# Kernel optimization log

Hardware: AMD Instinct MI355X
Metric: run time of the kernel (lower is better)

Reference implementation:

```python
import jax, jax.numpy as jnp
import numpy as np

NUM_CODES = 8192
LATENT_DIM = 256
BETA = 0.25
EPS_NORM = 1e-12  # F.normalize eps


def setup_inputs() -> dict:
    key = jax.random.key(0)
    k1, k2 = jax.random.split(key)
    z = jax.random.normal(k1, (8, LATENT_DIM, 32, 32), dtype=jnp.float32)
    # embedding initialized uniform(-1/K, 1/K); use that scale for realism
    codebook = jax.random.uniform(k2, (NUM_CODES, LATENT_DIM), dtype=jnp.float32,
                                  minval=-1.0 / NUM_CODES, maxval=1.0 / NUM_CODES)
    return {"z": z, "codebook": codebook}


def reference(z, codebook):
    # forward re-normalizes the codebook rows (F.normalize dim=1)
    norm = jnp.sqrt(jnp.sum(codebook * codebook, axis=1, keepdims=True))
    w = codebook / jnp.maximum(norm, EPS_NORM)                      # [K, D]

    z_perm = jnp.transpose(z, (0, 2, 3, 1))                          # [B, H, W, D]
    B, H, W, D = z_perm.shape
    zf = z_perm.reshape(-1, D)                                       # [N, D]

    # squared euclidean distances: ||z||^2 + ||w||^2 - 2 z w^T
    d = (jnp.sum(zf * zf, axis=1, keepdims=True)
         + jnp.sum(w * w, axis=1)
         - 2.0 * jnp.einsum('nd,kd->nk', zf, w))                     # [N, K]
    idx = jnp.argmin(d, axis=1)                                      # [N] int

    z_q = w[idx].reshape(B, H, W, D)                                 # gather

    # commitment + codebook loss
    loss = (jnp.mean((jax.lax.stop_gradient(z_q) - z_perm) ** 2)
            + BETA * jnp.mean((z_q - jax.lax.stop_gradient(z_perm)) ** 2))

    # straight-through estimator
    z_q = z_perm + jax.lax.stop_gradient(z_q - z_perm)

    # perplexity from codeword usage histogram (== mean of one-hots)
    N = idx.shape[0]
    counts = jnp.zeros((NUM_CODES,), dtype=jnp.float32).at[idx].add(1.0)
    avg_probs = counts / N
    perplexity = jnp.exp(-jnp.sum(avg_probs * jnp.log(avg_probs + 1e-10)))

    z_q = jnp.transpose(z_q, (0, 3, 1, 2))                           # back to NCHW
    return (z_q, idx, loss, perplexity)
```

## Files before the change

### kernel.cpp

```cpp
#include <hip/hip_runtime.h>
#include <hip/hip_bf16.h>
#include <math.h>

#define KC 8192
#define DD 256
#define NP 8192
#define ZQ_ELEMS 2097152
#define MARGIN_S 2.5e-4f
#define NPART 32

#define OFF_ABIG 0u
#define OFF_BBIG 8388608u
#define OFF_NRM  16777216u
#define OFF_WSQ  16809984u
#define OFF_PV1  16875520u
#define OFF_PV2  17924096u
#define OFF_PK1  18972672u
#define OFF_LOSSP 20021248u
#define OFF_HIST 20090880u
#define OFF_PACK 20123648u
#define OFF_LIST 20189184u
#define OFF_NFLG 20221952u

typedef __attribute__((ext_vector_type(8))) short bf16x8;
typedef __attribute__((ext_vector_type(4))) float f32x4;
typedef __attribute__((address_space(3))) void as3_void;
typedef const __attribute__((address_space(1))) void as1_cvoid;

#define GLOAD16(g, l) __builtin_amdgcn_global_load_lds((as1_cvoid*)(g), (as3_void*)(l), 16, 0, 0)

__device__ inline double waveReduceD(double v) {
#pragma unroll
    for (int off = 32; off; off >>= 1) v += __shfl_down(v, off, 64);
    return v;
}

static __device__ inline unsigned short f2bf(float f) {
    __hip_bfloat16 h = __float2bfloat16(f);
    return *(unsigned short*)&h;
}
static __device__ inline float bf2f(unsigned short u) {
    unsigned v = ((unsigned)u) << 16;
    float f;
    __builtin_memcpy(&f, &v, 4);
    return f;
}

__global__ __launch_bounds__(256) void prep(
    const float* __restrict__ cb, const float* __restrict__ z,
    unsigned short* __restrict__ Bbig, unsigned short* __restrict__ Abig,
    float* __restrict__ nrm, float* __restrict__ wsq,
    int* __restrict__ hist, int* __restrict__ nflag) {
    __shared__ float tile[64][65];
    int bid = blockIdx.x, t = threadIdx.x;
    int lane = t & 63, wid = t >> 6;
    if (bid < KC) {
        __shared__ double lred[4];
        __shared__ float mh;
        int k = bid;
        if (k < 32) hist[k * 256 + t] = 0;
        if (k == 32 && t == 0) *nflag = 0;
        float c = cb[k * DD + t];
        double s = waveReduceD((double)c * (double)c);
        if (lane == 0) lred[wid] = s;
        __syncthreads();
        if (t == 0) {
            double tot = lred[0] + lred[1] + lred[2] + lred[3];
            float nf = sqrtf((float)tot);
            mh = fmaxf(nf, 1e-12f);
            nrm[k] = mh;
            wsq[k] = (float)(tot / ((double)mh * (double)mh));
        }
        __syncthreads();
        float wv = c / mh;
        unsigned short hi = f2bf(wv);
        unsigned short lo = f2bf(wv - bf2f(hi));
        Bbig[k * 512 + t] = hi;
        Bbig[k * 512 + 256 + t] = lo;
    } else {
        int zb = bid - KC;
        int b = zb >> 6, ht = (zb >> 2) & 15, dt = zb & 3;
        int hw0 = ht * 64, d0 = dt * 64;
#pragma unroll
        for (int i = 0; i < 16; ++i) {
            int dl = wid * 16 + i;
            tile[dl][lane] = z[(size_t)(b * DD + d0 + dl) * 1024 + hw0 + lane];
        }
        __syncthreads();
#pragma unroll
        for (int i = 0; i < 16; ++i) {
            int nl = wid * 16 + i;
            float v = tile[lane][nl];
            unsigned short hi = f2bf(v);
            unsigned short lo = f2bf(v - bf2f(hi));
            size_t base = (size_t)(b * 1024 + hw0 + nl) * 512 + d0 + lane;
            Abig[base] = hi;
            Abig[base + 256] = lo;
        }
    }
}

__global__ __launch_bounds__(512, 2) void gemm_top2(
    const unsigned short* __restrict__ Abig, const unsigned short* __restrict__ Bbig,
    const float* __restrict__ wsq,
    float* __restrict__ pv1, float* __restrict__ pv2, int* __restrict__ pk1) {
    __shared__ unsigned short sAB[65536];

    int t = threadIdx.x;
    int l = t & 63, w = t >> 6;
    int wm = w >> 2, wn = w & 3;
    int kc0 = blockIdx.y * 256;
    int n0 = blockIdx.x * 256;

    int row0 = t >> 2;
    int lsw = (((t & 3) ^ ((row0 >> 1) & 3)) << 3);
    int subsw = (((l >> 4) ^ ((l >> 1) & 3)) << 3);

#define STAGE(kt_) do {                                                        \
    int p_ = (kt_) >> 3;                                                       \
    int zo_ = (p_ == 2 ? 256 : 0) + ((kt_) & 7) * 32;                          \
    int wo_ = (p_ == 1 ? 256 : 0) + ((kt_) & 7) * 32;                          \
    int b_ = ((kt_) & 3) * 16384;                                              \
    GLOAD16(Bbig + (size_t)(kc0 + row0) * 512 + wo_ + lsw, &sAB[b_ + t * 8]);  \
    GLOAD16(Bbig + (size_t)(kc0 + row0 + 128) * 512 + wo_ + lsw, &sAB[b_ + 4096 + t * 8]); \
    GLOAD16(Abig + (size_t)(n0 + row0) * 512 + zo_ + lsw, &sAB[b_ + 8192 + t * 8]); \
    GLOAD16(Abig + (size_t)(n0 + row0 + 128) * 512 + zo_ + lsw, &sAB[b_ + 12288 + t * 8]); \
} while (0)

#define LDFRAG(bufbase, fa, fb) do {                                           \
    _Pragma("unroll")                                                          \
    for (int mf = 0; mf < 8; ++mf)                                             \
        fa[mf] = *(const bf16x8*)&sAB[(bufbase) + (wm * 128 + mf * 16 + (l & 15)) * 32 + subsw]; \
    _Pragma("unroll")                                                          \
    for (int nf = 0; nf < 4; ++nf)                                             \
        fb[nf] = *(const bf16x8*)&sAB[(bufbase) + 8192 + (wn * 64 + nf * 16 + (l & 15)) * 32 + subsw]; \
} while (0)

#define MFMACL(fa, fb) do {                                                    \
    __builtin_amdgcn_s_setprio(1);                                             \
    _Pragma("unroll")                                                          \
    for (int mf = 0; mf < 8; ++mf)                                             \
        _Pragma("unroll")                                                      \
        for (int nf = 0; nf < 4; ++nf)                                         \
            acc[mf][nf] = __builtin_amdgcn_mfma_f32_16x16x32_bf16(fa[mf], fb[nf], acc[mf][nf], 0, 0, 0); \
    __builtin_amdgcn_s_setprio(0);                                             \
} while (0)

#define WAITBAR(n_) do {                                                       \
    asm volatile("s_waitcnt vmcnt(" #n_ ")" ::: "memory");                     \
    __builtin_amdgcn_s_barrier();                                              \
    asm volatile("" ::: "memory");                                             \
} while (0)

    f32x4 acc[8][4];
#pragma unroll
    for (int mf = 0; mf < 8; ++mf) {
#pragma unroll
        for (int r = 0; r < 4; ++r) {
            float hv = -0.5f * wsq[kc0 + wm * 128 + mf * 16 + ((l >> 4) << 2) + r];
#pragma unroll
            for (int nf = 0; nf < 4; ++nf) acc[mf][nf][r] = hv;
        }
    }

    bf16x8 fa0[8], fb0[4], fa1[8], fb1[4];

    STAGE(0);
    STAGE(1);
    STAGE(2);
    WAITBAR(8);
    LDFRAG(0, fa0, fb0);

    for (int kt = 0; kt < 20; kt += 2) {
        WAITBAR(4);
        LDFRAG(((kt + 1) & 3) * 16384, fa1, fb1);
        STAGE(kt + 3);
        MFMACL(fa0, fb0);
        WAITBAR(4);
        LDFRAG(((kt + 2) & 3) * 16384, fa0, fb0);
        STAGE(kt + 4);
        MFMACL(fa1, fb1);
    }
    WAITBAR(4);
    LDFRAG(1 * 16384, fa1, fb1);
    STAGE(23);
    MFMACL(fa0, fb0);
    WAITBAR(4);
    LDFRAG(2 * 16384, fa0, fb0);
    MFMACL(fa1, fb1);
    WAITBAR(0);
    LDFRAG(3 * 16384, fa1, fb1);
    MFMACL(fa0, fb0);
    MFMACL(fa1, fb1);

    float v1[4], v2[4];
    int k1[4];
#pragma unroll
    for (int nf = 0; nf < 4; ++nf) { v1[nf] = 3.4e38f; v2[nf] = 3.4e38f; k1[nf] = 0; }
#pragma unroll
    for (int mf = 0; mf < 8; ++mf) {
#pragma unroll
        for (int r = 0; r < 4; ++r) {
            int code = kc0 + wm * 128 + mf * 16 + ((l >> 4) << 2) + r;
#pragma unroll
            for (int nf = 0; nf < 4; ++nf) {
                float dv = -acc[mf][nf][r];
                bool lt = dv < v1[nf];
                v2[nf] = fminf(v2[nf], fmaxf(v1[nf], dv));
                v1[nf] = fminf(v1[nf], dv);
                k1[nf] = lt ? code : k1[nf];
            }
        }
    }
#pragma unroll
    for (int nf = 0; nf < 4; ++nf) {
#pragma unroll
        for (int mask = 16; mask <= 32; mask <<= 1) {
            float ov1 = __shfl_xor(v1[nf], mask, 64);
            float ov2 = __shfl_xor(v2[nf], mask, 64);
            int ok1 = __shfl_xor(k1[nf], mask, 64);
            bool take = (ov1 < v1[nf]) || (ov1 == v1[nf] && ok1 < k1[nf]);
            if (take) { v2[nf] = fminf(v1[nf], ov2); v1[nf] = ov1; k1[nf] = ok1; }
            else v2[nf] = fminf(v2[nf], ov1);
        }
    }
    __syncthreads();
    float* sv1 = (float*)sAB;
    float* sv2 = sv1 + 512;
    int* sk1 = (int*)(sv2 + 512);
    if ((l >> 4) == 0) {
#pragma unroll
        for (int nf = 0; nf < 4; ++nf) {
            int col = wn * 64 + nf * 16 + l;
            sv1[col * 2 + wm] = v1[nf];
            sv2[col * 2 + wm] = v2[nf];
            sk1[col * 2 + wm] = k1[nf];
        }
    }
    __syncthreads();
    if (t < 256) {
        float a1 = sv1[t * 2], b1 = sv1[t * 2 + 1];
        float a2 = sv2[t * 2], b2 = sv2[t * 2 + 1];
        int ak = sk1[t * 2], bk = sk1[t * 2 + 1];
        bool tb = (b1 < a1) || (b1 == a1 && bk < ak);
        float w1 = tb ? b1 : a1;
        int wk = tb ? bk : ak;
        float w2 = tb ? fminf(b2, a1) : fminf(a2, b1);
        pv1[blockIdx.y * NP + n0 + t] = w1;
        pv2[blockIdx.y * NP + n0 + t] = w2;
        pk1[blockIdx.y * NP + n0 + t] = wk;
    }
#undef STAGE
#undef LDFRAG
#undef MFMACL
#undef WAITBAR
}

__global__ __launch_bounds__(256) void merge_top2(
    const float* __restrict__ pv1, const float* __restrict__ pv2,
    const int* __restrict__ pk1, int* __restrict__ list, int* __restrict__ nflag,
    unsigned long long* __restrict__ packed) {
    int n = blockIdx.x * 256 + threadIdx.x;
    float gv1 = 3.4e38f, gv2 = 3.4e38f;
    int gk1 = 0;
#pragma unroll
    for (int ct = 0; ct < NPART; ++ct) {
        float v1 = pv1[ct * NP + n];
        if (v1 < gv1) {
            gv2 = fminf(gv1, pv2[ct * NP + n]);
            gv1 = v1;
            gk1 = pk1[ct * NP + n];
        } else {
            gv2 = fminf(gv2, v1);
        }
    }
    int f = (gv2 - gv1 < MARGIN_S) ? 1 : 0;
    packed[n] = f ? 0xFFFFFFFFFFFFFFFFull : (unsigned long long)(unsigned)gk1;
    if (f) {
        int pos = atomicAdd(nflag, 1);
        list[pos] = n;
    }
}

__global__ __launch_bounds__(256) void rescore_par(
    const float* __restrict__ z, const float* __restrict__ cb,
    const float* __restrict__ nrm, const float* __restrict__ wsq,
    const int* __restrict__ list, const int* __restrict__ nflag,
    unsigned long long* __restrict__ packed) {
    __shared__ float sz[256];
    int nf = *nflag;
    int t = threadIdx.x;
    int lane = t & 63, wv = t >> 6;
    for (int ii = blockIdx.x; ii < nf; ii += 64) {
        int n = list[ii];
        int b = n >> 10, hw = n & 1023;
        __syncthreads();
        sz[t] = z[(b * DD + t) * 1024 + hw];
        __syncthreads();
        float4 zr = ((const float4*)sz)[lane];
        double zqd = (double)zr.x * zr.x + (double)zr.y * zr.y
                   + (double)zr.z * zr.z + (double)zr.w * zr.w;
#pragma unroll
        for (int off = 32; off; off >>= 1) zqd += __shfl_xor(zqd, off, 64);
        float zq = (float)zqd;
        unsigned long long best = 0xFFFFFFFFFFFFFFFFull;
        int kbase = blockIdx.y * 256 + wv * 64;
        for (int j = 0; j < 64; ++j) {
            int k = kbase + j;
            float4 cc = *(const float4*)&cb[(size_t)k * DD + lane * 4];
            float p = (zr.x * cc.x + zr.y * cc.y) + (zr.z * cc.z + zr.w * cc.w);
#pragma unroll
            for (int off = 32; off; off >>= 1) p += __shfl_xor(p, off, 64);
            float dot = p / nrm[k];
            float dv = (zq + wsq[k]) - 2.0f * dot;
            unsigned bits = __float_as_uint(dv);
            bits = (bits & 0x80000000u) ? ~bits : (bits | 0x80000000u);
            unsigned long long pk = ((unsigned long long)bits << 32) | (unsigned)k;
            best = best < pk ? best : pk;
        }
        if (lane == 0) atomicMin(packed + n, best);
    }
}

__global__ __launch_bounds__(256) void gather_loss(
    const float* __restrict__ z, const float* __restrict__ cb,
    const float* __restrict__ nrm, const unsigned long long* __restrict__ packed,
    float* __restrict__ out, double* __restrict__ lossp, int* __restrict__ hist) {
    __shared__ double lred[4];
    int t = threadIdx.x;
    int base = (blockIdx.x * 256 + t) * 16;
    double s = 0.0;
#pragma unroll
    for (int q = 0; q < 4; ++q) {
        int e = base + q * 4;
        int b = e >> 18, d = (e >> 10) & 255, hw = e & 1023;
        int n = (b << 10) + hw;
        float4 zv = *(const float4*)&z[e];
        float o[4];
        int ks[4];
#pragma unroll
        for (int j = 0; j < 4; ++j) {
            ks[j] = (int)(packed[n + j] & 0xFFFFFFFFull);
            o[j] = cb[ks[j] * DD + d] / nrm[ks[j]];
        }
        *(float4*)&out[e] = make_float4(o[0], o[1], o[2], o[3]);
        if (d == 0) {
#pragma unroll
            for (int j = 0; j < 4; ++j) {
                out[ZQ_ELEMS + n + j] = (float)ks[j];
                atomicAdd(&hist[ks[j]], 1);
            }
        }
        float d0 = o[0] - zv.x, d1 = o[1] - zv.y, d2 = o[2] - zv.z, d3 = o[3] - zv.w;
        s += (double)(d0 * d0) + (double)(d1 * d1) + (double)(d2 * d2) + (double)(d3 * d3);
    }
    s = waveReduceD(s);
    int lane = t & 63, wid = t >> 6;
    if (lane == 0) lred[wid] = s;
    __syncthreads();
    if (t == 0) lossp[blockIdx.x] = lred[0] + lred[1] + lred[2] + lred[3];
}

__global__ __launch_bounds__(256) void finalize_kernel(
    const int* __restrict__ hist, const double* __restrict__ lossp,
    float* __restrict__ out) {
    __shared__ double lred[4];
    __shared__ double lsum;
    int t = threadIdx.x;
    int lane = t & 63, wid = t >> 6;
    double ls = lossp[t] + lossp[t + 256];
    ls = waveReduceD(ls);
    if (lane == 0) lred[wid] = ls;
    __syncthreads();
    if (t == 0) lsum = lred[0] + lred[1] + lred[2] + lred[3];
    __syncthreads();
    double s = 0.0;
    for (int i = t; i < KC; i += 256) {
        float p = (float)hist[i] * (1.0f / 8192.0f);
        float lg = logf(p + 1e-10f);
        s += (double)(p * lg);
    }
    s = waveReduceD(s);
    if (lane == 0) lred[wid] = s;
    __syncthreads();
    if (t == 0) {
        double tot = lred[0] + lred[1] + lred[2] + lred[3];
        float m = (float)(lsum / (double)ZQ_ELEMS);
        out[ZQ_ELEMS + NP] = m + 0.25f * m;
        out[ZQ_ELEMS + NP + 1] = expf(-(float)tot);
    }
}

extern "C" void kernel_launch(void* const* d_in, const int* in_sizes, int n_in,
                              void* d_out, int out_size, void* d_ws, size_t ws_size,
                              hipStream_t stream) {
    const float* z = (const float*)d_in[0];
    const float* cb = (const float*)d_in[1];
    float* out = (float*)d_out;
    char* ws = (char*)d_ws;

    unsigned short* Abig = (unsigned short*)(ws + OFF_ABIG);
    unsigned short* Bbig = (unsigned short*)(ws + OFF_BBIG);
    float* nrm = (float*)(ws + OFF_NRM);
    float* wsq = (float*)(ws + OFF_WSQ);
    float* pv1 = (float*)(ws + OFF_PV1);
    float* pv2 = (float*)(ws + OFF_PV2);
    int* pk1 = (int*)(ws + OFF_PK1);
    int* hist = (int*)(ws + OFF_HIST);
    double* lossp = (double*)(ws + OFF_LOSSP);
    unsigned long long* packed = (unsigned long long*)(ws + OFF_PACK);
    int* list = (int*)(ws + OFF_LIST);
    int* nflag = (int*)(ws + OFF_NFLG);

    prep<<<KC + 512, 256, 0, stream>>>(cb, z, Bbig, Abig, nrm, wsq, hist, nflag);
    gemm_top2<<<dim3(32, NPART), 512, 0, stream>>>(Abig, Bbig, wsq, pv1, pv2, pk1);
    merge_top2<<<NP / 256, 256, 0, stream>>>(pv1, pv2, pk1, list, nflag, packed);
    rescore_par<<<dim3(64, 32), 256, 0, stream>>>(z, cb, nrm, wsq, list, nflag, packed);
    gather_loss<<<ZQ_ELEMS / (256 * 16), 256, 0, stream>>>(z, cb, nrm, packed, out, lossp, hist);
    finalize_kernel<<<1, 256, 0, stream>>>(hist, lossp, out);
}
```

Measured before the change: 207.5 us.

## Merge top-2 partials with 64-bit atomics and fuse finalize into gather

The GEMM epilogue now folds each block's top-1/top-2 candidates straight into per-row 64-bit atomicMin slots, using a monotone float-to-uint key. This removes the separate merge kernel and the partial-result buffers. Rescore now reads the ambiguity flag itself instead of using a compacted list. The finalize kernel is folded into the gather kernel with a last-block-done counter. Prep also handles four codebook rows per block, one wave each, with vectorized loads and stores. Together these cut two kernel launches and some global traffic, at the cost of atomic contention in the GEMM epilogue and a per-block scan over all rows in rescore.

```diff
diff --git a/kernel.cpp b/kernel.cpp
--- a/kernel.cpp
+++ b/kernel.cpp
@@ -7,20 +7,17 @@
 #define NP 8192
 #define ZQ_ELEMS 2097152
 #define MARGIN_S 2.5e-4f
-#define NPART 32
 
 #define OFF_ABIG 0u
 #define OFF_BBIG 8388608u
 #define OFF_NRM  16777216u
 #define OFF_WSQ  16809984u
-#define OFF_PV1  16875520u
-#define OFF_PV2  17924096u
-#define OFF_PK1  18972672u
-#define OFF_LOSSP 20021248u
-#define OFF_HIST 20090880u
-#define OFF_PACK 20123648u
-#define OFF_LIST 20189184u
-#define OFF_NFLG 20221952u
+#define OFF_P    16842752u
+#define OFF_P2   16908288u
+#define OFF_R    16973824u
+#define OFF_LOSSP 17039360u
+#define OFF_HIST 17043456u
+#define OFF_DONE 17076224u
 
 typedef __attribute__((ext_vector_type(8))) short bf16x8;
 typedef __attribute__((ext_vector_type(4))) float f32x4;
@@ -45,40 +42,52 @@
     __builtin_memcpy(&f, &v, 4);
     return f;
 }
+static __device__ inline unsigned mono(float f) {
+    unsigned b = __float_as_uint(f);
+    return (b & 0x80000000u) ? ~b : (b | 0x80000000u);
+}
+static __device__ inline float invmono(unsigned u) {
+    unsigned b = (u & 0x80000000u) ? (u & 0x7FFFFFFFu) : ~u;
+    return __uint_as_float(b);
+}
 
 __global__ __launch_bounds__(256) void prep(
     const float* __restrict__ cb, const float* __restrict__ z,
     unsigned short* __restrict__ Bbig, unsigned short* __restrict__ Abig,
-    float* __restrict__ nrm, float* __restrict__ wsq,
-    int* __restrict__ hist, int* __restrict__ nflag) {
-    __shared__ float tile[64][65];
+    float* __restrict__ nrm, float* __restrict__ wsq, int* __restrict__ hist,
+    unsigned long long* __restrict__ P, unsigned long long* __restrict__ P2,
+    unsigned long long* __restrict__ R, unsigned int* __restrict__ done) {
     int bid = blockIdx.x, t = threadIdx.x;
     int lane = t & 63, wid = t >> 6;
-    if (bid < KC) {
-        __shared__ double lred[4];
-        __shared__ float mh;
-        int k = bid;
-        if (k < 32) hist[k * 256 + t] = 0;
-        if (k == 32 && t == 0) *nflag = 0;
-        float c = cb[k * DD + t];
-        double s = waveReduceD((double)c * (double)c);
-        if (lane == 0) lred[wid] = s;
-        __syncthreads();
-        if (t == 0) {
-            double tot = lred[0] + lred[1] + lred[2] + lred[3];
-            float nf = sqrtf((float)tot);
-            mh = fmaxf(nf, 1e-12f);
+    if (bid < 2048) {
+        if (bid < 32) hist[bid * 256 + t] = 0;
+        if (bid == 32 && t == 0) *done = 0u;
+        int k = bid * 4 + wid;
+        float4 c4 = *(const float4*)&cb[(size_t)k * DD + lane * 4];
+        double s = (double)c4.x * c4.x + (double)c4.y * c4.y
+                 + (double)c4.z * c4.z + (double)c4.w * c4.w;
+#pragma unroll
+        for (int off = 32; off; off >>= 1) s += __shfl_xor(s, off, 64);
+        float mh = fmaxf(sqrtf((float)s), 1e-12f);
+        if (lane == 0) {
             nrm[k] = mh;
-            wsq[k] = (float)(tot / ((double)mh * (double)mh));
-        }
-        __syncthreads();
-        float wv = c / mh;
-        unsigned short hi = f2bf(wv);
-        unsigned short lo = f2bf(wv - bf2f(hi));
-        Bbig[k * 512 + t] = hi;
-        Bbig[k * 512 + 256 + t] = lo;
+            wsq[k] = (float)(s / ((double)mh * (double)mh));
+            P[k] = 0xFFFFFFFFFFFFFFFFull;
+            P2[k] = 0xFFFFFFFFFFFFFFFFull;
+            R[k] = 0xFFFFFFFFFFFFFFFFull;
+        }
+        float wv[4] = {c4.x / mh, c4.y / mh, c4.z / mh, c4.w / mh};
+        unsigned short hi[4], lo[4];
+#pragma unroll
+        for (int j = 0; j < 4; ++j) {
+            hi[j] = f2bf(wv[j]);
+            lo[j] = f2bf(wv[j] - bf2f(hi[j]));
+        }
+        *(ushort4*)&Bbig[(size_t)k * 512 + lane * 4] = make_ushort4(hi[0], hi[1], hi[2], hi[3]);
+        *(ushort4*)&Bbig[(size_t)k * 512 + 256 + lane * 4] = make_ushort4(lo[0], lo[1], lo[2], lo[3]);
     } else {
-        int zb = bid - KC;
+        __shared__ float tile[64][65];
+        int zb = bid - 2048;
         int b = zb >> 6, ht = (zb >> 2) & 15, dt = zb & 3;
         int hw0 = ht * 64, d0 = dt * 64;
 #pragma unroll
@@ -103,7 +112,7 @@
 __global__ __launch_bounds__(512, 2) void gemm_top2(
     const unsigned short* __restrict__ Abig, const unsigned short* __restrict__ Bbig,
     const float* __restrict__ wsq,
-    float* __restrict__ pv1, float* __restrict__ pv2, int* __restrict__ pk1) {
+    unsigned long long* __restrict__ P, unsigned long long* __restrict__ P2) {
     __shared__ unsigned short sAB[65536];
 
     int t = threadIdx.x;
@@ -246,9 +255,11 @@
         float w1 = tb ? b1 : a1;
         int wk = tb ? bk : ak;
         float w2 = tb ? fminf(b2, a1) : fminf(a2, b1);
-        pv1[blockIdx.y * NP + n0 + t] = w1;
-        pv2[blockIdx.y * NP + n0 + t] = w2;
-        pk1[blockIdx.y * NP + n0 + t] = wk;
+        int n = n0 + t;
+        unsigned long long x = ((unsigned long long)mono(w1) << 32) | (unsigned)wk;
+        unsigned long long old = atomicMin(&P[n], x);
+        atomicMin(&P2[n], old > x ? old : x);
+        atomicMin(&P2[n], ((unsigned long long)mono(w2) << 32) | 0xFFFFFFFFull);
     }
 #undef STAGE
 #undef LDFRAG
@@ -256,43 +267,25 @@
 #undef WAITBAR
 }
 
-__global__ __launch_bounds__(256) void merge_top2(
-    const float* __restrict__ pv1, const float* __restrict__ pv2,
-    const int* __restrict__ pk1, int* __restrict__ list, int* __restrict__ nflag,
-    unsigned long long* __restrict__ packed) {
-    int n = blockIdx.x * 256 + threadIdx.x;
-    float gv1 = 3.4e38f, gv2 = 3.4e38f;
-    int gk1 = 0;
-#pragma unroll
-    for (int ct = 0; ct < NPART; ++ct) {
-        float v1 = pv1[ct * NP + n];
-        if (v1 < gv1) {
-            gv2 = fminf(gv1, pv2[ct * NP + n]);
-            gv1 = v1;
-            gk1 = pk1[ct * NP + n];
-        } else {
-            gv2 = fminf(gv2, v1);
-        }
-    }
-    int f = (gv2 - gv1 < MARGIN_S) ? 1 : 0;
-    packed[n] = f ? 0xFFFFFFFFFFFFFFFFull : (unsigned long long)(unsigned)gk1;
-    if (f) {
-        int pos = atomicAdd(nflag, 1);
-        list[pos] = n;
-    }
-}
-
 __global__ __launch_bounds__(256) void rescore_par(
     const float* __restrict__ z, const float* __restrict__ cb,
     const float* __restrict__ nrm, const float* __restrict__ wsq,
-    const int* __restrict__ list, const int* __restrict__ nflag,
-    unsigned long long* __restrict__ packed) {
+    const unsigned long long* __restrict__ P, const unsigned long long* __restrict__ P2,
+    unsigned long long* __restrict__ R) {
     __shared__ float sz[256];
-    int nf = *nflag;
+    __shared__ unsigned char fl[128];
     int t = threadIdx.x;
     int lane = t & 63, wv = t >> 6;
-    for (int ii = blockIdx.x; ii < nf; ii += 64) {
-        int n = list[ii];
+    if (t < 128) {
+        int n = blockIdx.x + t * 64;
+        float s1 = invmono((unsigned)(P[n] >> 32));
+        float s2 = invmono((unsigned)(P2[n] >> 32));
+        fl[t] = (s2 - s1 < MARGIN_S) ? 1 : 0;
+    }
+    __syncthreads();
+    for (int ii = 0; ii < 128; ++ii) {
+        if (!fl[ii]) continue;
+        int n = blockIdx.x + ii * 64;
         int b = n >> 10, hw = n & 1023;
         __syncthreads();
         sz[t] = z[(b * DD + t) * 1024 + hw];
@@ -313,21 +306,25 @@
             for (int off = 32; off; off >>= 1) p += __shfl_xor(p, off, 64);
             float dot = p / nrm[k];
             float dv = (zq + wsq[k]) - 2.0f * dot;
-            unsigned bits = __float_as_uint(dv);
-            bits = (bits & 0x80000000u) ? ~bits : (bits | 0x80000000u);
-            unsigned long long pk = ((unsigned long long)bits << 32) | (unsigned)k;
+            unsigned long long pk = ((unsigned long long)mono(dv) << 32) | (unsigned)k;
             best = best < pk ? best : pk;
         }
-        if (lane == 0) atomicMin(packed + n, best);
-    }
-}
-
-__global__ __launch_bounds__(256) void gather_loss(
+        if (lane == 0) atomicMin(&R[n], best);
+    }
+}
+
+__global__ __launch_bounds__(256) void gather_fin(
     const float* __restrict__ z, const float* __restrict__ cb,
-    const float* __restrict__ nrm, const unsigned long long* __restrict__ packed,
-    float* __restrict__ out, double* __restrict__ lossp, int* __restrict__ hist) {
+    const float* __restrict__ nrm,
+    const unsigned long long* __restrict__ P, const unsigned long long* __restrict__ P2,
+    const unsigned long long* __restrict__ R,
+    float* __restrict__ out, double* __restrict__ lossp, int* __restrict__ hist,
+    unsigned int* __restrict__ done) {
     __shared__ double lred[4];
+    __shared__ int amLast;
+    __shared__ double lsum;
     int t = threadIdx.x;
+    int lane = t & 63, wid = t >> 6;
     int base = (blockIdx.x * 256 + t) * 16;
     double s = 0.0;
 #pragma unroll
@@ -340,7 +337,11 @@
         int ks[4];
 #pragma unroll
         for (int j = 0; j < 4; ++j) {
-            ks[j] = (int)(packed[n + j] & 0xFFFFFFFFull);
+            unsigned long long p = P[n + j];
+            float s1 = invmono((unsigned)(p >> 32));
+            float s2 = invmono((unsigned)(P2[n + j] >> 32));
+            unsigned long long wnr = (s2 - s1 < MARGIN_S) ? R[n + j] : p;
+            ks[j] = (int)(wnr & 0xFFFFFFFFull);
             o[j] = cb[ks[j] * DD + d] / nrm[ks[j]];
         }
         *(float4*)&out[e] = make_float4(o[0], o[1], o[2], o[3]);
@@ -355,39 +356,36 @@
         s += (double)(d0 * d0) + (double)(d1 * d1) + (double)(d2 * d2) + (double)(d3 * d3);
     }
     s = waveReduceD(s);
-    int lane = t & 63, wid = t >> 6;
     if (lane == 0) lred[wid] = s;
     __syncthreads();
     if (t == 0) lossp[blockIdx.x] = lred[0] + lred[1] + lred[2] + lred[3];
-}
-
-__global__ __launch_bounds__(256) void finalize_kernel(
-    const int* __restrict__ hist, const double* __restrict__ lossp,
-    float* __restrict__ out) {
-    __shared__ double lred[4];
-    __shared__ double lsum;
-    int t = threadIdx.x;
-    int lane = t & 63, wid = t >> 6;
-    double ls = lossp[t] + lossp[t + 256];
-    ls = waveReduceD(ls);
-    if (lane == 0) lred[wid] = ls;
-    __syncthreads();
-    if (t == 0) lsum = lred[0] + lred[1] + lred[2] + lred[3];
-    __syncthreads();
-    double s = 0.0;
-    for (int i = t; i < KC; i += 256) {
-        float p = (float)hist[i] * (1.0f / 8192.0f);
-        float lg = logf(p + 1e-10f);
-        s += (double)(p * lg);
-    }
-    s = waveReduceD(s);
-    if (lane == 0) lred[wid] = s;
-    __syncthreads();
-    if (t == 0) {
-        double tot = lred[0] + lred[1] + lred[2] + lred[3];
-        float m = (float)(lsum / (double)ZQ_ELEMS);
-        out[ZQ_ELEMS + NP] = m + 0.25f * m;
-        out[ZQ_ELEMS + NP + 1] = expf(-(float)tot);
+    __threadfence();
+    __syncthreads();
+    if (t == 0) amLast = (atomicAdd(done, 1u) == (unsigned)(gridDim.x - 1)) ? 1 : 0;
+    __syncthreads();
+    if (amLast) {
+        __threadfence();
+        double ls = lossp[t] + lossp[t + 256];
+        ls = waveReduceD(ls);
+        if (lane == 0) lred[wid] = ls;
+        __syncthreads();
+        if (t == 0) lsum = lred[0] + lred[1] + lred[2] + lred[3];
+        __syncthreads();
+        double ps = 0.0;
+        for (int i = t; i < KC; i += 256) {
+            float p = (float)hist[i] * (1.0f / 8192.0f);
+            float lg = logf(p + 1e-10f);
+            ps += (double)(p * lg);
+        }
+        ps = waveReduceD(ps);
+        if (lane == 0) lred[wid] = ps;
+        __syncthreads();
+        if (t == 0) {
+            double tot = lred[0] + lred[1] + lred[2] + lred[3];
+            float m = (float)(lsum / (double)ZQ_ELEMS);
+            out[ZQ_ELEMS + NP] = m + 0.25f * m;
+            out[ZQ_ELEMS + NP + 1] = expf(-(float)tot);
+        }
     }
 }
 
@@ -403,19 +401,15 @@
     unsigned short* Bbig = (unsigned short*)(ws + OFF_BBIG);
     float* nrm = (float*)(ws + OFF_NRM);
     float* wsq = (float*)(ws + OFF_WSQ);
-    float* pv1 = (float*)(ws + OFF_PV1);
-    float* pv2 = (float*)(ws + OFF_PV2);
-    int* pk1 = (int*)(ws + OFF_PK1);
+    unsigned long long* P = (unsigned long long*)(ws + OFF_P);
+    unsigned long long* P2 = (unsigned long long*)(ws + OFF_P2);
+    unsigned long long* R = (unsigned long long*)(ws + OFF_R);
+    double* lossp = (double*)(ws + OFF_LOSSP);
     int* hist = (int*)(ws + OFF_HIST);
-    double* lossp = (double*)(ws + OFF_LOSSP);
-    unsigned long long* packed = (unsigned long long*)(ws + OFF_PACK);
-    int* list = (int*)(ws + OFF_LIST);
-    int* nflag = (int*)(ws + OFF_NFLG);
-
-    prep<<<KC + 512, 256, 0, stream>>>(cb, z, Bbig, Abig, nrm, wsq, hist, nflag);
-    gemm_top2<<<dim3(32, NPART), 512, 0, stream>>>(Abig, Bbig, wsq, pv1, pv2, pk1);
-    merge_top2<<<NP / 256, 256, 0, stream>>>(pv1, pv2, pk1, list, nflag, packed);
-    rescore_par<<<dim3(64, 32), 256, 0, stream>>>(z, cb, nrm, wsq, list, nflag, packed);
-    gather_loss<<<ZQ_ELEMS / (256 * 16), 256, 0, stream>>>(z, cb, nrm, packed, out, lossp, hist);
-    finalize_kernel<<<1, 256, 0, stream>>>(hist, lossp, out);
-}
+    unsigned int* done = (unsigned int*)(ws + OFF_DONE);
+
+    prep<<<2560, 256, 0, stream>>>(cb, z, Bbig, Abig, nrm, wsq, hist, P, P2, R, done);
+    gemm_top2<<<dim3(32, 32), 512, 0, stream>>>(Abig, Bbig, wsq, P, P2);
+    rescore_par<<<dim3(64, 32), 256, 0, stream>>>(z, cb, nrm, wsq, P, P2, R);
+    gather_fin<<<512, 256, 0, stream>>>(z, cb, nrm, P, P2, R, out, lossp, hist, done);
+}
```

Result: slower. 293.7 us (+41.6%).

## Loop each GEMM block over four code tiles and vectorize codebook prep

Applied to the files above, without the earlier changes.

The gemm_top2 grid shrinks from 32 to 8 code partitions. Each block now sweeps 1024 codes in one continuous pipelined loop, taking a running top-2 between code tiles, and the partial results are stored row-major per point for the merge. The prep kernel handles four codebook rows per block, one per wave, using float4 loads and shuffle reductions instead of one row per 256-thread block. This cuts block count, per-block pipeline prologue and epilogue overhead, and merge traffic, but leaves fewer blocks (256) to fill the GPU, which may hurt occupancy and load balance.

```diff
diff --git a/kernel.cpp b/kernel.cpp
--- a/kernel.cpp
+++ b/kernel.cpp
@@ -7,7 +7,7 @@
 #define NP 8192
 #define ZQ_ELEMS 2097152
 #define MARGIN_S 2.5e-4f
-#define NPART 32
+#define NPART 8
 
 #define OFF_ABIG 0u
 #define OFF_BBIG 8388608u
@@ -51,34 +51,34 @@
     unsigned short* __restrict__ Bbig, unsigned short* __restrict__ Abig,
     float* __restrict__ nrm, float* __restrict__ wsq,
     int* __restrict__ hist, int* __restrict__ nflag) {
-    __shared__ float tile[64][65];
     int bid = blockIdx.x, t = threadIdx.x;
     int lane = t & 63, wid = t >> 6;
-    if (bid < KC) {
-        __shared__ double lred[4];
-        __shared__ float mh;
-        int k = bid;
-        if (k < 32) hist[k * 256 + t] = 0;
-        if (k == 32 && t == 0) *nflag = 0;
-        float c = cb[k * DD + t];
-        double s = waveReduceD((double)c * (double)c);
-        if (lane == 0) lred[wid] = s;
-        __syncthreads();
-        if (t == 0) {
-            double tot = lred[0] + lred[1] + lred[2] + lred[3];
-            float nf = sqrtf((float)tot);
-            mh = fmaxf(nf, 1e-12f);
+    if (bid < 2048) {
+        if (bid < 32) hist[bid * 256 + t] = 0;
+        if (bid == 32 && t == 0) *nflag = 0;
+        int k = bid * 4 + wid;
+        float4 c4 = *(const float4*)&cb[(size_t)k * DD + lane * 4];
+        double s = (double)c4.x * c4.x + (double)c4.y * c4.y
+                 + (double)c4.z * c4.z + (double)c4.w * c4.w;
+#pragma unroll
+        for (int off = 32; off; off >>= 1) s += __shfl_xor(s, off, 64);
+        float mh = fmaxf(sqrtf((float)s), 1e-12f);
+        if (lane == 0) {
             nrm[k] = mh;
-            wsq[k] = (float)(tot / ((double)mh * (double)mh));
-        }
-        __syncthreads();
-        float wv = c / mh;
-        unsigned short hi = f2bf(wv);
-        unsigned short lo = f2bf(wv - bf2f(hi));
-        Bbig[k * 512 + t] = hi;
-        Bbig[k * 512 + 256 + t] = lo;
+            wsq[k] = (float)(s / ((double)mh * (double)mh));
+        }
+        float wv[4] = {c4.x / mh, c4.y / mh, c4.z / mh, c4.w / mh};
+        unsigned short hi[4], lo[4];
+#pragma unroll
+        for (int j = 0; j < 4; ++j) {
+            hi[j] = f2bf(wv[j]);
+            lo[j] = f2bf(wv[j] - bf2f(hi[j]));
+        }
+        *(ushort4*)&Bbig[(size_t)k * 512 + lane * 4] = make_ushort4(hi[0], hi[1], hi[2], hi[3]);
+        *(ushort4*)&Bbig[(size_t)k * 512 + 256 + lane * 4] = make_ushort4(lo[0], lo[1], lo[2], lo[3]);
     } else {
-        int zb = bid - KC;
+        __shared__ float tile[64][65];
+        int zb = bid - 2048;
         int b = zb >> 6, ht = (zb >> 2) & 15, dt = zb & 3;
         int hw0 = ht * 64, d0 = dt * 64;
 #pragma unroll
@@ -109,20 +109,23 @@
     int t = threadIdx.x;
     int l = t & 63, w = t >> 6;
     int wm = w >> 2, wn = w & 3;
-    int kc0 = blockIdx.y * 256;
+    int kc0 = blockIdx.y * 1024;
     int n0 = blockIdx.x * 256;
 
     int row0 = t >> 2;
     int lsw = (((t & 3) ^ ((row0 >> 1) & 3)) << 3);
     int subsw = (((l >> 4) ^ ((l >> 1) & 3)) << 3);
 
-#define STAGE(kt_) do {                                                        \
-    int p_ = (kt_) >> 3;                                                       \
-    int zo_ = (p_ == 2 ? 256 : 0) + ((kt_) & 7) * 32;                          \
-    int wo_ = (p_ == 1 ? 256 : 0) + ((kt_) & 7) * 32;                          \
-    int b_ = ((kt_) & 3) * 16384;                                              \
-    GLOAD16(Bbig + (size_t)(kc0 + row0) * 512 + wo_ + lsw, &sAB[b_ + t * 8]);  \
-    GLOAD16(Bbig + (size_t)(kc0 + row0 + 128) * 512 + wo_ + lsw, &sAB[b_ + 4096 + t * 8]); \
+#define STAGE(g_) do {                                                         \
+    int ct_ = (g_) / 24;                                                       \
+    int kt_ = (g_) % 24;                                                       \
+    int p_ = kt_ >> 3;                                                         \
+    int zo_ = (p_ == 2 ? 256 : 0) + (kt_ & 7) * 32;                            \
+    int wo_ = (p_ == 1 ? 256 : 0) + (kt_ & 7) * 32;                            \
+    int b_ = ((g_) & 3) * 16384;                                               \
+    int kc_ = kc0 + ct_ * 256;                                                 \
+    GLOAD16(Bbig + (size_t)(kc_ + row0) * 512 + wo_ + lsw, &sAB[b_ + t * 8]);  \
+    GLOAD16(Bbig + (size_t)(kc_ + row0 + 128) * 512 + wo_ + lsw, &sAB[b_ + 4096 + t * 8]); \
     GLOAD16(Abig + (size_t)(n0 + row0) * 512 + zo_ + lsw, &sAB[b_ + 8192 + t * 8]); \
     GLOAD16(Abig + (size_t)(n0 + row0 + 128) * 512 + zo_ + lsw, &sAB[b_ + 12288 + t * 8]); \
 } while (0)
@@ -152,16 +155,43 @@
     asm volatile("" ::: "memory");                                             \
 } while (0)
 
+#define RESETACC(ct_) do {                                                     \
+    _Pragma("unroll")                                                          \
+    for (int mf = 0; mf < 8; ++mf) {                                           \
+        _Pragma("unroll")                                                      \
+        for (int r = 0; r < 4; ++r) {                                          \
+            float hv = -0.5f * wsq[kc0 + (ct_) * 256 + wm * 128 + mf * 16 + ((l >> 4) << 2) + r]; \
+            _Pragma("unroll")                                                  \
+            for (int nf = 0; nf < 4; ++nf) acc[mf][nf][r] = hv;                \
+        }                                                                      \
+    }                                                                          \
+} while (0)
+
+#define EXTRACT(ct_) do {                                                      \
+    _Pragma("unroll")                                                          \
+    for (int mf = 0; mf < 8; ++mf) {                                           \
+        _Pragma("unroll")                                                      \
+        for (int r = 0; r < 4; ++r) {                                          \
+            int code = kc0 + (ct_) * 256 + wm * 128 + mf * 16 + ((l >> 4) << 2) + r; \
+            _Pragma("unroll")                                                  \
+            for (int nf = 0; nf < 4; ++nf) {                                   \
+                float dv = -acc[mf][nf][r];                                    \
+                bool lt = dv < v1[nf];                                         \
+                v2[nf] = fminf(v2[nf], fmaxf(v1[nf], dv));                     \
+                v1[nf] = fminf(v1[nf], dv);                                    \
+                k1[nf] = lt ? code : k1[nf];                                   \
+            }                                                                  \
+        }                                                                      \
+    }                                                                          \
+} while (0)
+
+    float v1[4], v2[4];
+    int k1[4];
+#pragma unroll
+    for (int nf = 0; nf < 4; ++nf) { v1[nf] = 3.4e38f; v2[nf] = 3.4e38f; k1[nf] = 0; }
+
     f32x4 acc[8][4];
-#pragma unroll
-    for (int mf = 0; mf < 8; ++mf) {
-#pragma unroll
-        for (int r = 0; r < 4; ++r) {
-            float hv = -0.5f * wsq[kc0 + wm * 128 + mf * 16 + ((l >> 4) << 2) + r];
-#pragma unroll
-            for (int nf = 0; nf < 4; ++nf) acc[mf][nf][r] = hv;
-        }
-    }
+    RESETACC(0);
 
     bf16x8 fa0[8], fb0[4], fa1[8], fb1[4];
 
@@ -171,47 +201,27 @@
     WAITBAR(8);
     LDFRAG(0, fa0, fb0);
 
-    for (int kt = 0; kt < 20; kt += 2) {
+    for (int g = 0; g < 94; g += 2) {
         WAITBAR(4);
-        LDFRAG(((kt + 1) & 3) * 16384, fa1, fb1);
-        STAGE(kt + 3);
+        LDFRAG(((g + 1) & 3) * 16384, fa1, fb1);
+        STAGE(g + 3);
         MFMACL(fa0, fb0);
         WAITBAR(4);
-        LDFRAG(((kt + 2) & 3) * 16384, fa0, fb0);
-        STAGE(kt + 4);
+        LDFRAG(((g + 2) & 3) * 16384, fa0, fb0);
+        if (g < 92) STAGE(g + 4);
         MFMACL(fa1, fb1);
-    }
-    WAITBAR(4);
-    LDFRAG(1 * 16384, fa1, fb1);
-    STAGE(23);
-    MFMACL(fa0, fb0);
-    WAITBAR(4);
-    LDFRAG(2 * 16384, fa0, fb0);
-    MFMACL(fa1, fb1);
+        if (((g + 1) % 24) == 23) {
+            int ct = (g + 1) / 24;
+            EXTRACT(ct);
+            RESETACC(ct + 1);
+        }
+    }
     WAITBAR(0);
     LDFRAG(3 * 16384, fa1, fb1);
     MFMACL(fa0, fb0);
     MFMACL(fa1, fb1);
-
-    float v1[4], v2[4];
-    int k1[4];
-#pragma unroll
-    for (int nf = 0; nf < 4; ++nf) { v1[nf] = 3.4e38f; v2[nf] = 3.4e38f; k1[nf] = 0; }
-#pragma unroll
-    for (int mf = 0; mf < 8; ++mf) {
-#pragma unroll
-        for (int r = 0; r < 4; ++r) {
-            int code = kc0 + wm * 128 + mf * 16 + ((l >> 4) << 2) + r;
-#pragma unroll
-            for (int nf = 0; nf < 4; ++nf) {
-                float dv = -acc[mf][nf][r];
-                bool lt = dv < v1[nf];
-                v2[nf] = fminf(v2[nf], fmaxf(v1[nf], dv));
-                v1[nf] = fminf(v1[nf], dv);
-                k1[nf] = lt ? code : k1[nf];
-            }
-        }
-    }
+    EXTRACT(3);
+
 #pragma unroll
     for (int nf = 0; nf < 4; ++nf) {
 #pragma unroll
@@ -246,14 +256,16 @@
         float w1 = tb ? b1 : a1;
         int wk = tb ? bk : ak;
         float w2 = tb ? fminf(b2, a1) : fminf(a2, b1);
-        pv1[blockIdx.y * NP + n0 + t] = w1;
-        pv2[blockIdx.y * NP + n0 + t] = w2;
-        pk1[blockIdx.y * NP + n0 + t] = wk;
+        pv1[(size_t)(n0 + t) * NPART + blockIdx.y] = w1;
+        pv2[(size_t)(n0 + t) * NPART + blockIdx.y] = w2;
+        pk1[(size_t)(n0 + t) * NPART + blockIdx.y] = wk;
     }
 #undef STAGE
 #undef LDFRAG
 #undef MFMACL
 #undef WAITBAR
+#undef RESETACC
+#undef EXTRACT
 }
 
 __global__ __launch_bounds__(256) void merge_top2(
@@ -265,11 +277,11 @@
     int gk1 = 0;
 #pragma unroll
     for (int ct = 0; ct < NPART; ++ct) {
-        float v1 = pv1[ct * NP + n];
+        float v1 = pv1[(size_t)n * NPART + ct];
         if (v1 < gv1) {
-            gv2 = fminf(gv1, pv2[ct * NP + n]);
+            gv2 = fminf(gv1, pv2[(size_t)n * NPART + ct]);
             gv1 = v1;
-            gk1 = pk1[ct * NP + n];
+            gk1 = pk1[(size_t)n * NPART + ct];
         } else {
             gv2 = fminf(gv2, v1);
         }
@@ -412,7 +424,7 @@
     int* list = (int*)(ws + OFF_LIST);
     int* nflag = (int*)(ws + OFF_NFLG);
 
-    prep<<<KC + 512, 256, 0, stream>>>(cb, z, Bbig, Abig, nrm, wsq, hist, nflag);
+    prep<<<2560, 256, 0, stream>>>(cb, z, Bbig, Abig, nrm, wsq, hist, nflag);
     gemm_top2<<<dim3(32, NPART), 512, 0, stream>>>(Abig, Bbig, wsq, pv1, pv2, pk1);
     merge_top2<<<NP / 256, 256, 0, stream>>>(pv1, pv2, pk1, list, nflag, packed);
     rescore_par<<<dim3(64, 32), 256, 0, stream>>>(z, cb, nrm, wsq, list, nflag, packed);
```

New measurement: 186.3 us. 1.11x faster.
